# Kernel tuning notes

Measured on AMD Instinct MI355X. Metric: run time of the kernel, lower is better.

Reference implementation:

```python
import jax, jax.numpy as jnp
import numpy as np

B, D, N, H = 2, 1024, 2048, 16
Da = D // H
NEG = -1e30


def setup_inputs() -> dict:
    key = jax.random.key(0)
    k1, k2, k3, k4, k5 = jax.random.split(key, 5)
    x = jax.random.normal(k1, (B, D, N), dtype=jnp.float32)
    mask = jnp.ones((B, N), dtype=jnp.float32)
    s = 1.0 / np.sqrt(D)
    Wq = jax.random.normal(k2, (H, D, Da), dtype=jnp.float32) * s
    Wk = jax.random.normal(k3, (H, D, Da), dtype=jnp.float32) * s
    Wv = jax.random.normal(k4, (H, D, Da), dtype=jnp.float32) * s
    Wo = jax.random.normal(k5, (D, D), dtype=jnp.float32) * s
    return {"x": x, "mask": mask, "Wq": Wq, "Wk": Wk, "Wv": Wv, "Wo": Wo}


def reference(x, mask, Wq, Wk, Wv, Wo):
    # x: [B, D, N] -> [B, N, D]
    xt = jnp.swapaxes(x, 1, 2)
    scale = 1.0 / np.sqrt(Da)
    # per-head projections, batched over heads: [B, H, N, Da]
    q = jnp.einsum("bnd,hde->bhne", xt, Wq)
    k = jnp.einsum("bnd,hde->bhne", xt, Wk)
    v = jnp.einsum("bnd,hde->bhne", xt, Wv)
    # scaled scores: [B, H, N, N]
    scores = jnp.einsum("bhne,bhme->bhnm", q, k) * scale
    hmask = mask[:, None, None, :]  # additive mask over keys
    vmask = mask[:, None, :, None]  # multiplicative mask over queries
    scores = scores * hmask + (1.0 - hmask) * NEG
    attn = jax.nn.softmax(scores, axis=-1) * vmask
    heads = jnp.einsum("bhnm,bhme->bhne", attn, v)
    # concat heads along feature dim: [B, N, H*Da]
    head = jnp.swapaxes(heads, 1, 2).reshape(xt.shape[0], xt.shape[1], H * Da)
    out = head @ Wo  # [B, N, D]
    return jnp.swapaxes(out, 1, 2)  # [B, D, N]
```

## Files before the change

kernel.cpp:

```cpp
#include <hip/hip_runtime.h>

typedef _Float16 f16;
typedef _Float16 f16x4 __attribute__((ext_vector_type(4)));
typedef _Float16 f16x8 __attribute__((ext_vector_type(8)));
typedef __fp16 fp16x2 __attribute__((ext_vector_type(2)));
typedef float f32x4 __attribute__((ext_vector_type(4)));
typedef float f32x16 __attribute__((ext_vector_type(16)));
typedef int i32x4 __attribute__((ext_vector_type(4)));

#define NEGV (-1e30f)
#define MBASE 10.0f

#if __has_builtin(__builtin_amdgcn_exp2f)
#define EXP2(x) __builtin_amdgcn_exp2f(x)
#else
#define EXP2(x) exp2f(x)
#endif

__device__ __forceinline__ void gload16(const f16* g, f16* l) {
  __builtin_amdgcn_global_load_lds(
      (const __attribute__((address_space(1))) void*)g,
      (__attribute__((address_space(3))) void*)l, 16, 0, 0);
}

__device__ __forceinline__ int pkh(float a, float b) {
  fp16x2 p = __builtin_amdgcn_cvt_pkrtz(a, b);
  return __builtin_bit_cast(int, p);
}

__device__ __forceinline__ void plswap(int& a, int& b) {
#if __has_builtin(__builtin_amdgcn_permlane32_swap)
  auto r = __builtin_amdgcn_permlane32_swap(a, b, false, false);
  a = r[0];
  b = r[1];
#else
  int an = __shfl_xor(b, 32);
  int bn = __shfl_xor(a, 32);
  bool lo = (threadIdx.x & 63) < 32;
  int a2 = lo ? a : an;
  int b2 = lo ? bn : b;
  a = a2;
  b = b2;
#endif
}

__global__ __launch_bounds__(256) void prep_kernel(
    const float* __restrict__ x, const float* __restrict__ Wq,
    const float* __restrict__ Wk, const float* __restrict__ Wv,
    const float* __restrict__ Wo, f16* __restrict__ xt,
    f16* __restrict__ WqkvT, f16* __restrict__ WoT)
{
  __shared__ float t[32][33];
  int tx = threadIdx.x & 31, ty = threadIdx.x >> 5;
  int id = blockIdx.x;
  const float* src;
  f16* dst;
  int a0, b0, sld;
  float sc = 1.0f;
  if (id < 4096) {
    int b = id >> 11, rem = id & 2047;
    a0 = (rem >> 6) * 32;
    b0 = (rem & 63) * 32;
    sld = 2048;
    src = x + (size_t)b * 1024 * 2048;
    dst = xt + (size_t)b * 2048 * 1024;
  } else if (id < 7168) {
    int i = id - 4096;
    a0 = (i & 31) * 32;
    b0 = ((i >> 5) & 1) * 32;
    int z = i >> 6, m = z >> 4, h = z & 15;
    sld = 64;
    src = ((m == 0) ? Wq : (m == 1) ? Wk : Wv) + (size_t)h * 65536;
    sc = (m == 0) ? 0.18033688011112042f : 1.0f;
    dst = WqkvT + (size_t)(m * 1024 + h * 64) * 1024;
  } else {
    int i = id - 7168;
    a0 = (i >> 5) * 32;
    b0 = (i & 31) * 32;
    sld = 1024;
    src = Wo;
    dst = WoT;
  }
#pragma unroll
  for (int i = 0; i < 4; ++i)
    t[ty + 8 * i][tx] = src[(size_t)(a0 + ty + 8 * i) * sld + b0 + tx] * sc;
  __syncthreads();
#pragma unroll
  for (int i = 0; i < 4; ++i)
    dst[(size_t)(b0 + ty + 8 * i) * 1024 + a0 + tx] = (f16)t[tx][ty + 8 * i];
}

template <int BN>
__global__ __launch_bounds__(512, 4) void gemm_f16_kernel(
    const f16* __restrict__ A, const f16* __restrict__ Bt,
    int K, int ldc, long bstride, long cstride,
    f16* __restrict__ Ch, float* __restrict__ Cf,
    const float* __restrict__ rowmask, int mcol0,
    f16* __restrict__ Vt)
{
  const int NACC = BN / 64;
  __shared__ __align__(16) f16 smem[32768];
  f16* As = smem;
  f16* Bs = smem + 16384;

  int tid = threadIdx.x;
  int lane = tid & 63, w = tid >> 6, g = lane >> 4, r = lane & 15;
  int wr = w >> 2, wc = w & 3;

  int nbx = gridDim.x;
  int n = nbx * gridDim.y;
  int flat = blockIdx.y * nbx + blockIdx.x;
  int nf = (flat & 7) * (n >> 3) + (flat >> 3);
  int bx = nf % nbx, by = nf / nbx;

  size_t row0 = (size_t)by * 128;
  size_t col0 = (size_t)bx * BN;
  Bt += (size_t)blockIdx.z * (size_t)bstride;

  int l8 = lane >> 3;
  int sseg = ((lane & 7) ^ l8) * 8;
  int r7 = r & 7;

  f32x4 acc[4][NACC];
#pragma unroll
  for (int m = 0; m < 4; ++m)
#pragma unroll
    for (int nn = 0; nn < NACC; ++nn)
      acc[m][nn] = (f32x4){0.f, 0.f, 0.f, 0.f};

  const f16* Ap = A + (row0 + w * 16 + l8) * (size_t)K + sseg;
  const f16* Bp;
  if (BN == 128)
    Bp = Bt + (col0 + w * 16 + l8) * (size_t)K + sseg;
  else
    Bp = Bt + (col0 + w * 8 + l8) * (size_t)K + sseg;

  auto stage = [&](int nb, int k0) {
#pragma unroll
    for (int i = 0; i < 2; ++i)
      gload16(Ap + (size_t)i * 8 * K + k0, As + nb * 8192 + w * 1024 + i * 512);
    if (BN == 128) {
#pragma unroll
      for (int i = 0; i < 2; ++i)
        gload16(Bp + (size_t)i * 8 * K + k0, Bs + nb * 8192 + w * 1024 + i * 512);
    } else {
      gload16(Bp + k0, Bs + nb * 8192 + w * 512);
    }
  };

  stage(0, 0);
  __syncthreads();

  for (int k0 = 0; k0 < K; k0 += 64) {
    int cur = (k0 >> 6) & 1;
    if (k0 + 64 < K) stage(cur ^ 1, k0 + 64);
    const f16* Ac = As + cur * 8192;
    const f16* Bc = Bs + cur * 8192;
#pragma unroll
    for (int j = 0; j < 2; ++j) {
      f16x8 af[4], bf[NACC];
      int tseg = j * 4 + g;
#pragma unroll
      for (int m = 0; m < 4; ++m)
        af[m] = *(const f16x8*)&Ac[(wr * 64 + m * 16 + r) * 64 + ((tseg ^ r7) << 3)];
#pragma unroll
      for (int nn = 0; nn < NACC; ++nn) {
        int brow = (BN == 128) ? (wc * 32 + nn * 16 + r) : (wc * 16 + r);
        bf[nn] = *(const f16x8*)&Bc[brow * 64 + ((tseg ^ r7) << 3)];
      }
#pragma unroll
      for (int m = 0; m < 4; ++m)
#pragma unroll
        for (int nn = 0; nn < NACC; ++nn)
          acc[m][nn] = __builtin_amdgcn_mfma_f32_16x16x32_f16(af[m], bf[nn], acc[m][nn], 0, 0, 0);
    }
    __syncthreads();
  }

  if (BN == 128 && Vt && col0 >= 2048) {
    int b = (int)(row0 >> 11);
    int n0 = (int)(row0 & 2047);
    int vcol0 = (int)col0 - 2048;
#pragma unroll
    for (int h2 = 0; h2 < 2; ++h2) {
      if ((wc >> 1) == h2) {
        int wcl = wc & 1;
#pragma unroll
        for (int m = 0; m < 4; ++m)
#pragma unroll
          for (int nn = 0; nn < NACC; ++nn) {
            int cl = wcl * 32 + nn * 16 + r;
            int row = wr * 64 + m * 16 + g * 4;
            int rowp = row ^ ((cl & 7) << 3);
            f16x4 v4 = {(f16)acc[m][nn][0], (f16)acc[m][nn][1],
                        (f16)acc[m][nn][2], (f16)acc[m][nn][3]};
            *(f16x4*)&smem[cl * 128 + rowp] = v4;
          }
      }
      __syncthreads();
#pragma unroll
      for (int ii = 0; ii < 2; ++ii) {
        int chunk = ii * 512 + tid;
        int el = chunk >> 4, seg = chunk & 15;
        int rowp = (seg * 8) ^ ((el & 7) << 3);
        f16x8 v8 = *(const f16x8*)&smem[el * 128 + rowp];
        *(f16x8*)&Vt[(size_t)(b * 1024 + vcol0 + h2 * 64 + el) * 2048 + n0 + seg * 8] = v8;
      }
      __syncthreads();
    }
  } else if (Ch) {
    Ch += (size_t)blockIdx.z * (size_t)cstride;
#pragma unroll
    for (int m = 0; m < 4; ++m)
#pragma unroll
      for (int nn = 0; nn < NACC; ++nn)
#pragma unroll
        for (int q = 0; q < 4; ++q) {
          size_t row = row0 + wr * 64 + m * 16 + g * 4 + q;
          int col = (int)col0 + ((BN == 128) ? (wc * 32 + nn * 16 + r) : (wc * 16 + r));
          float v = acc[m][nn][q];
          if (rowmask && col >= mcol0) v *= rowmask[row];
          Ch[row * (size_t)ldc + col] = (f16)v;
        }
  } else {
    Cf += (size_t)blockIdx.z * (size_t)cstride;
#pragma unroll
    for (int m = 0; m < 4; ++m)
#pragma unroll
      for (int nn = 0; nn < NACC; ++nn)
#pragma unroll
        for (int q = 0; q < 4; ++q) {
          int col = (int)col0 + ((BN == 128) ? (wc * 32 + nn * 16 + r) : (wc * 16 + r));
          Cf[(row0 + wr * 64 + m * 16 + g * 4 + q) * (size_t)ldc + col] = acc[m][nn][q];
        }
  }
}

__global__ __launch_bounds__(512, 4) void attn_kernel(const f16* __restrict__ qk,
                                                      const f16* __restrict__ Vt,
                                                      const float* __restrict__ mask,
                                                      f16* __restrict__ head)
{
  __shared__ __align__(16) f16 smem[16384];
  __shared__ __align__(16) f16 negcH[2048];
  __shared__ __align__(16) float ll[8][32];
  __shared__ __align__(16) float il[2][32];
  __shared__ int aflag;

  int tid = threadIdx.x;
  int w = tid >> 6, lane = tid & 63;
  int l31 = lane & 31, hb = lane >> 5;
  int hb4 = hb * 4;
  int wq = w >> 2, wk = w & 3;

  int flat = blockIdx.x;
  int nf = (flat & 7) * 128 + (flat >> 3);
  int qt = nf & 31, bh = nf >> 5;
  int b = bh >> 4, hh = bh & 15;
  const float* maskb = mask + b * 2048;

  if (tid == 0) aflag = 0;
  __syncthreads();

  {
    const float* mp = maskb + tid * 4;
    f32x4 m0 = *(const f32x4*)(mp);
    int localany = 0;
#pragma unroll
    for (int j = 0; j < 4; ++j) {
      negcH[tid * 4 + j] = (f16)((1.0f - m0[j]) * -60000.0f);
      localany |= (m0[j] != 1.0f);
    }
    if (localany) aflag = 1;
  }

  int qrow = qt * 64 + wq * 32 + l31;
  const f16* qp = qk + ((size_t)(b * 2048 + qrow)) * 2048 + hh * 64;
  f16x8 qf[4];
#pragma unroll
  for (int ec = 0; ec < 4; ++ec)
    qf[ec] = *(const f16x8*)(qp + ec * 16 + hb * 8);

  const f16* kg0 = qk + ((size_t)(b * 2048)) * 2048 + 1024 + hh * 64;
  const f16* vg0 = Vt + ((size_t)((b * 16 + hh) * 64)) * 2048;

  int ksrow = tid >> 3, kseg = tid & 7;
  int ks2 = (kseg ^ (ksrow & 7)) * 8;
  int vsrow = tid >> 4, vseg2 = tid & 15;
  int vs2 = (vseg2 ^ (vsrow & 7)) * 8;

  auto stage = [&](int kt_) {
    const f16* kg = kg0 + (size_t)kt_ * 128 * 2048;
    const f16* vg = vg0 + kt_ * 128;
    gload16(kg + (size_t)ksrow * 2048 + ks2, smem + w * 512);
    gload16(kg + (size_t)(ksrow + 64) * 2048 + ks2, smem + 4096 + w * 512);
    gload16(vg + (size_t)vsrow * 2048 + vs2, smem + 8192 + w * 512);
    gload16(vg + (size_t)(vsrow + 32) * 2048 + vs2, smem + 12288 + w * 512);
  };

  __syncthreads();
  const bool anymask = (aflag != 0);

  f32x16 zc;
#pragma unroll
  for (int i = 0; i < 16; ++i) zc[i] = 0.f;
  f32x16 o0 = zc, o1 = zc;
  float lrun = 0.f;

  int kb0 = (wk * 32 + l31) * 64;
  int k7 = l31 & 7;
  int vb0 = l31 * 128, vb1 = vb0 + 4096;

  for (int kt = 0; kt < 16; ++kt) {
    stage(kt);
    __syncthreads();

    const f16* Kc = smem;
    const f16* Vc = smem + 8192;

    f32x16 s = zc;
    if (anymask) {
      const f16* nb = &negcH[kt * 128 + wk * 32];
#pragma unroll
      for (int rr = 0; rr < 4; ++rr)
#pragma unroll
        for (int j = 0; j < 4; ++j)
          s[rr * 4 + j] = (float)nb[rr * 8 + hb4 + j];
    }
    __builtin_amdgcn_s_setprio(1);
#pragma unroll
    for (int ec = 0; ec < 4; ++ec) {
      int so = ((((ec << 1) | hb) ^ k7) << 3);
      f16x8 kf = *(const f16x8*)&Kc[kb0 + so];
      s = __builtin_amdgcn_mfma_f32_32x32x16_f16(kf, qf[ec], s, 0, 0, 0);
    }
    __builtin_amdgcn_s_setprio(0);

#pragma unroll
    for (int i = 0; i < 16; ++i) s[i] = EXP2(s[i] - MBASE);
    float b2[8];
#pragma unroll
    for (int i = 0; i < 8; ++i) b2[i] = s[i] + s[i + 8];
#pragma unroll
    for (int stp = 4; stp > 0; stp >>= 1)
#pragma unroll
      for (int i = 0; i < stp; ++i) b2[i] += b2[i + stp];
    lrun += b2[0];

    __builtin_amdgcn_s_setprio(1);
#pragma unroll
    for (int kc = 0; kc < 2; ++kc) {
      int t0a = pkh(s[kc * 8 + 0], s[kc * 8 + 1]);
      int t0b = pkh(s[kc * 8 + 2], s[kc * 8 + 3]);
      int t1a = pkh(s[kc * 8 + 4], s[kc * 8 + 5]);
      int t1b = pkh(s[kc * 8 + 6], s[kc * 8 + 7]);
      plswap(t0a, t1a);
      plswap(t0b, t1b);
      f16x8 af = __builtin_bit_cast(f16x8, (i32x4){t0a, t0b, t1a, t1b});
      int vseg = wk * 4 + kc * 2 + hb;
      int vs = ((vseg ^ k7) << 3);
      f16x8 vf0 = *(const f16x8*)&Vc[vb0 + vs];
      f16x8 vf1 = *(const f16x8*)&Vc[vb1 + vs];
      o0 = __builtin_amdgcn_mfma_f32_32x32x16_f16(af, vf0, o0, 0, 0, 0);
      o1 = __builtin_amdgcn_mfma_f32_32x32x16_f16(af, vf1, o1, 0, 0, 0);
    }
    __builtin_amdgcn_s_setprio(0);

    __syncthreads();
  }

  lrun += __shfl_xor(lrun, 32);
  if (hb == 0) ll[w][l31] = lrun;
  __syncthreads();
  if (wk == 0 && hb == 0) {
    float lt = ll[w][l31] + ll[w + 1][l31] + ll[w + 2][l31] + ll[w + 3][l31];
    il[wq][l31] = maskb[qrow] / lt;
  }
  float* scr = (float*)smem;
  if (wk & 1) {
    float* sp = scr + (wq * 2 + (wk >> 1)) * 2048;
#pragma unroll
    for (int i = 0; i < 16; ++i) {
      sp[i * 64 + lane] = o0[i];
      sp[(16 + i) * 64 + lane] = o1[i];
    }
  }
  __syncthreads();
  if (!(wk & 1)) {
    float* sp = scr + (wq * 2 + (wk >> 1)) * 2048;
#pragma unroll
    for (int i = 0; i < 16; ++i) {
      o0[i] += sp[i * 64 + lane];
      o1[i] += sp[(16 + i) * 64 + lane];
    }
  }
  __syncthreads();
  if (wk == 2) {
    float* sp = scr + wq * 2048;
#pragma unroll
    for (int i = 0; i < 16; ++i) {
      sp[i * 64 + lane] = o0[i];
      sp[(16 + i) * 64 + lane] = o1[i];
    }
  }
  __syncthreads();
  if (wk == 0) {
    float* sp = scr + wq * 2048;
#pragma unroll
    for (int i = 0; i < 16; ++i) {
      o0[i] += sp[i * 64 + lane];
      o1[i] += sp[(16 + i) * 64 + lane];
    }
    f16* hp = head + ((size_t)(b * 2048 + qt * 64 + wq * 32)) * 1024 + hh * 64 + l31;
#pragma unroll
    for (int rr = 0; rr < 4; ++rr) {
      f32x4 iv = *(const f32x4*)&il[wq][rr * 8 + hb4];
#pragma unroll
      for (int j = 0; j < 4; ++j) {
        int crow = j + rr * 8 + hb4;
        hp[(size_t)crow * 1024] = (f16)(o0[rr * 4 + j] * iv[j]);
        hp[(size_t)crow * 1024 + 32] = (f16)(o1[rr * 4 + j] * iv[j]);
      }
    }
  }
}

extern "C" void kernel_launch(void* const* d_in, const int* in_sizes, int n_in,
                              void* d_out, int out_size, void* d_ws, size_t ws_size,
                              hipStream_t stream)
{
  const float* x    = (const float*)d_in[0];
  const float* mask = (const float*)d_in[1];
  const float* Wq   = (const float*)d_in[2];
  const float* Wk   = (const float*)d_in[3];
  const float* Wv   = (const float*)d_in[4];
  const float* Wo   = (const float*)d_in[5];
  float* out = (float*)d_out;

  char* ws = (char*)d_ws;
  f16* xt_head = (f16*)(ws);
  f16* WqkvT   = (f16*)(ws + 8388608);
  f16* WoT     = (f16*)(ws + 14680064);
  f16* qk      = (f16*)(ws + 16777216);
  f16* Vt      = (f16*)(ws + 33554432);

  prep_kernel<<<dim3(8192), 256, 0, stream>>>(x, Wq, Wk, Wv, Wo, xt_head, WqkvT, WoT);

  gemm_f16_kernel<128><<<dim3(24, 32, 1), 512, 0, stream>>>(
      xt_head, WqkvT, 1024, 2048, 0, 0, qk, nullptr, mask, 1024, Vt);

  attn_kernel<<<dim3(1024), 512, 0, stream>>>(qk, Vt, mask, xt_head);

  gemm_f16_kernel<64><<<dim3(32, 8, 2), 512, 0, stream>>>(
      WoT, xt_head, 1024, 2048, (long)2048 * 1024, (long)1024 * 2048, nullptr, out,
      nullptr, 0, nullptr);
}
```

Baseline: 128.6 us.

## Double-buffer K/V tiles in attention and halve block to four waves

The attention kernel now runs with 256 threads (2 query waves by 2 key waves) instead of 512. It walks 32 key tiles of 64 keys each, and uses double-buffered LDS so the next tile's global-to-LDS load is issued before the current tile is computed. This is meant to overlap the K/V transfer with the MFMA work and to remove one stage of the cross-wave output reduction. The mask preprocessing is moved after the first prefetch. The trade-off is fewer waves per block and more loop iterations per wave, which may reduce latency hiding across waves.

```diff
diff --git a/kernel.cpp b/kernel.cpp
--- a/kernel.cpp
+++ b/kernel.cpp
@@ -236,14 +236,14 @@
   }
 }
 
-__global__ __launch_bounds__(512, 4) void attn_kernel(const f16* __restrict__ qk,
+__global__ __launch_bounds__(256, 4) void attn_kernel(const f16* __restrict__ qk,
                                                       const f16* __restrict__ Vt,
                                                       const float* __restrict__ mask,
                                                       f16* __restrict__ head)
 {
   __shared__ __align__(16) f16 smem[16384];
   __shared__ __align__(16) f16 negcH[2048];
-  __shared__ __align__(16) float ll[8][32];
+  __shared__ __align__(16) float ll[4][32];
   __shared__ __align__(16) float il[2][32];
   __shared__ int aflag;
 
@@ -251,7 +251,7 @@
   int w = tid >> 6, lane = tid & 63;
   int l31 = lane & 31, hb = lane >> 5;
   int hb4 = hb * 4;
-  int wq = w >> 2, wk = w & 3;
+  int wq = w >> 1, wk = w & 1;
 
   int flat = blockIdx.x;
   int nf = (flat & 7) * 128 + (flat >> 3);
@@ -260,19 +260,6 @@
   const float* maskb = mask + b * 2048;
 
   if (tid == 0) aflag = 0;
-  __syncthreads();
-
-  {
-    const float* mp = maskb + tid * 4;
-    f32x4 m0 = *(const f32x4*)(mp);
-    int localany = 0;
-#pragma unroll
-    for (int j = 0; j < 4; ++j) {
-      negcH[tid * 4 + j] = (f16)((1.0f - m0[j]) * -60000.0f);
-      localany |= (m0[j] != 1.0f);
-    }
-    if (localany) aflag = 1;
-  }
 
   int qrow = qt * 64 + wq * 32 + l31;
   const f16* qp = qk + ((size_t)(b * 2048 + qrow)) * 2048 + hh * 64;
@@ -284,20 +271,37 @@
   const f16* kg0 = qk + ((size_t)(b * 2048)) * 2048 + 1024 + hh * 64;
   const f16* vg0 = Vt + ((size_t)((b * 16 + hh) * 64)) * 2048;
 
-  int ksrow = tid >> 3, kseg = tid & 7;
-  int ks2 = (kseg ^ (ksrow & 7)) * 8;
-  int vsrow = tid >> 4, vseg2 = tid & 15;
-  int vs2 = (vseg2 ^ (vsrow & 7)) * 8;
-
-  auto stage = [&](int kt_) {
-    const f16* kg = kg0 + (size_t)kt_ * 128 * 2048;
-    const f16* vg = vg0 + kt_ * 128;
-    gload16(kg + (size_t)ksrow * 2048 + ks2, smem + w * 512);
-    gload16(kg + (size_t)(ksrow + 64) * 2048 + ks2, smem + 4096 + w * 512);
-    gload16(vg + (size_t)vsrow * 2048 + vs2, smem + 8192 + w * 512);
-    gload16(vg + (size_t)(vsrow + 32) * 2048 + vs2, smem + 12288 + w * 512);
+  int srow = tid >> 3;
+  int sseg = tid & 7;
+  int s2 = (sseg ^ (srow & 7)) * 8;
+
+  auto stage = [&](int nb, int kt_) {
+    const f16* kg = kg0 + (size_t)kt_ * 64 * 2048;
+    const f16* vg = vg0 + kt_ * 64;
+    f16* Kd = smem + nb * 4096;
+    f16* Vd = smem + 8192 + nb * 4096;
+    gload16(kg + (size_t)srow * 2048 + s2, Kd + w * 512);
+    gload16(kg + (size_t)(srow + 32) * 2048 + s2, Kd + 2048 + w * 512);
+    gload16(vg + (size_t)srow * 2048 + s2, Vd + w * 512);
+    gload16(vg + (size_t)(srow + 32) * 2048 + s2, Vd + 2048 + w * 512);
   };
 
+  stage(0, 0);
+  __syncthreads();
+
+  {
+    const float* mp = maskb + tid * 8;
+    f32x4 m0 = *(const f32x4*)(mp);
+    f32x4 m1 = *(const f32x4*)(mp + 4);
+    int localany = 0;
+#pragma unroll
+    for (int j = 0; j < 4; ++j) {
+      negcH[tid * 8 + j] = (f16)((1.0f - m0[j]) * -60000.0f);
+      negcH[tid * 8 + 4 + j] = (f16)((1.0f - m1[j]) * -60000.0f);
+      localany |= (m0[j] != 1.0f) | (m1[j] != 1.0f);
+    }
+    if (localany) aflag = 1;
+  }
   __syncthreads();
   const bool anymask = (aflag != 0);
 
@@ -309,18 +313,18 @@
 
   int kb0 = (wk * 32 + l31) * 64;
   int k7 = l31 & 7;
-  int vb0 = l31 * 128, vb1 = vb0 + 4096;
-
-  for (int kt = 0; kt < 16; ++kt) {
-    stage(kt);
-    __syncthreads();
-
-    const f16* Kc = smem;
-    const f16* Vc = smem + 8192;
+  int vb0 = l31 * 64, vb1 = vb0 + 2048;
+
+  for (int kt = 0; kt < 32; ++kt) {
+    int cur = kt & 1;
+    if (kt + 1 < 32) stage(cur ^ 1, kt + 1);
+
+    const f16* Kc = smem + cur * 4096;
+    const f16* Vc = smem + 8192 + cur * 4096;
 
     f32x16 s = zc;
     if (anymask) {
-      const f16* nb = &negcH[kt * 128 + wk * 32];
+      const f16* nb = &negcH[kt * 64 + wk * 32];
 #pragma unroll
       for (int rr = 0; rr < 4; ++rr)
 #pragma unroll
@@ -357,8 +361,7 @@
       plswap(t0a, t1a);
       plswap(t0b, t1b);
       f16x8 af = __builtin_bit_cast(f16x8, (i32x4){t0a, t0b, t1a, t1b});
-      int vseg = wk * 4 + kc * 2 + hb;
-      int vs = ((vseg ^ k7) << 3);
+      int vs = (((wk * 4 + (kc << 1)) | hb) ^ k7) << 3;
       f16x8 vf0 = *(const f16x8*)&Vc[vb0 + vs];
       f16x8 vf1 = *(const f16x8*)&Vc[vb1 + vs];
       o0 = __builtin_amdgcn_mfma_f32_32x32x16_f16(af, vf0, o0, 0, 0, 0);
@@ -373,29 +376,11 @@
   if (hb == 0) ll[w][l31] = lrun;
   __syncthreads();
   if (wk == 0 && hb == 0) {
-    float lt = ll[w][l31] + ll[w + 1][l31] + ll[w + 2][l31] + ll[w + 3][l31];
+    float lt = ll[w][l31] + ll[w + 1][l31];
     il[wq][l31] = maskb[qrow] / lt;
   }
   float* scr = (float*)smem;
-  if (wk & 1) {
-    float* sp = scr + (wq * 2 + (wk >> 1)) * 2048;
-#pragma unroll
-    for (int i = 0; i < 16; ++i) {
-      sp[i * 64 + lane] = o0[i];
-      sp[(16 + i) * 64 + lane] = o1[i];
-    }
-  }
-  __syncthreads();
-  if (!(wk & 1)) {
-    float* sp = scr + (wq * 2 + (wk >> 1)) * 2048;
-#pragma unroll
-    for (int i = 0; i < 16; ++i) {
-      o0[i] += sp[i * 64 + lane];
-      o1[i] += sp[(16 + i) * 64 + lane];
-    }
-  }
-  __syncthreads();
-  if (wk == 2) {
+  if (wk == 1) {
     float* sp = scr + wq * 2048;
 #pragma unroll
     for (int i = 0; i < 16; ++i) {
@@ -449,7 +434,7 @@
   gemm_f16_kernel<128><<<dim3(24, 32, 1), 512, 0, stream>>>(
       xt_head, WqkvT, 1024, 2048, 0, 0, qk, nullptr, mask, 1024, Vt);
 
-  attn_kernel<<<dim3(1024), 512, 0, stream>>>(qk, Vt, mask, xt_head);
+  attn_kernel<<<dim3(1024), 256, 0, stream>>>(qk, Vt, mask, xt_head);
 
   gemm_f16_kernel<64><<<dim3(32, 8, 2), 512, 0, stream>>>(
       WoT, xt_head, 1024, 2048, (long)2048 * 1024, (long)1024 * 2048, nullptr, out,
```

New measurement: 124.9 us. 1.03x faster.
